# Kernel optimization log

Hardware: AMD Instinct MI355X
Metric: run time of the kernel (lower is better)

Reference implementation:

```python
import jax, jax.numpy as jnp
import numpy as np

D = 1024

def setup_inputs() -> dict:
    key = jax.random.key(0)
    ks = jax.random.split(key, 12)
    sc_in = 1.0 / np.sqrt(D)
    sc_in2 = 1.0 / np.sqrt(2 * D)
    inp = {
        "X1": jax.random.normal(ks[0], (8, D), dtype=jnp.float32),
        "X2": jax.random.normal(ks[1], (8, 2048, D), dtype=jnp.float32),
        # Linear params: weight stored as [in, out], bias [out]
        "Wq1": jax.random.normal(ks[2], (D, D), dtype=jnp.float32) * sc_in,
        "bq1": jax.random.normal(ks[3], (D,), dtype=jnp.float32) * 0.01,
        "Wq2": jax.random.normal(ks[4], (D, D), dtype=jnp.float32) * sc_in,
        "bq2": jax.random.normal(ks[5], (D,), dtype=jnp.float32) * 0.01,
        "Wk1": jax.random.normal(ks[6], (D, D), dtype=jnp.float32) * sc_in,
        "bk1": jax.random.normal(ks[7], (D,), dtype=jnp.float32) * 0.01,
        "Wk2": jax.random.normal(ks[8], (D, D), dtype=jnp.float32) * sc_in,
        "bk2": jax.random.normal(ks[9], (D,), dtype=jnp.float32) * 0.01,
        "Wv": jax.random.normal(ks[10], (2 * D, D), dtype=jnp.float32) * sc_in2,
        "bv": jax.random.normal(ks[11], (D,), dtype=jnp.float32) * 0.01,
        "alpha": jnp.float32(0.5),
    }
    return inp

def reference(X1, X2, Wq1, bq1, Wq2, bq2, Wk1, bk1, Wk2, bk2, Wv, bv, alpha):
    B, S, Dm = X2.shape
    # broadcast X1 [B, D] -> [B, S, D]
    X1e = jnp.broadcast_to(X1[:, None, :], (B, S, Dm))
    X = jnp.concatenate([X1e, X2], axis=-1)  # [B, S, 2D]
    Q1 = X1e @ Wq1 + bq1
    K1 = X1e @ Wk1 + bk1
    Q2 = X2 @ Wq2 + bq2
    K2 = X2 @ Wk2 + bk2
    V = X @ Wv + bv  # [B, S, D]
    s = 1.0 / jnp.sqrt(jnp.float32(Dm))
    A1 = jnp.einsum('bqd,bkd->bqk', Q1, K1) * s
    A2 = jnp.einsum('bqd,bkd->bqk', Q2, K2) * s
    A = jax.nn.softmax(A2, axis=-1) - alpha * jax.nn.softmax(A1, axis=-1)
    return jnp.einsum('bqk,bkd->bqd', A, V)
```

## Files before the change

### kernel.cpp

```cpp
#include <hip/hip_runtime.h>

typedef unsigned short u16;
typedef unsigned int u32;
typedef __bf16 bf16x8 __attribute__((ext_vector_type(8)));
typedef float f32x4 __attribute__((ext_vector_type(4)));
typedef u16 u16x4 __attribute__((ext_vector_type(4)));
typedef u16 u16x8 __attribute__((ext_vector_type(8)));

#define MFMA16(a,b,c) __builtin_amdgcn_mfma_f32_16x16x32_bf16((a),(b),(c),0,0,0)

__device__ __forceinline__ u16 f2bf(float f) {
  u32 u = __builtin_bit_cast(u32, f);
  u += 0x7fffu + ((u >> 16) & 1u);
  return (u16)(u >> 16);
}
__device__ __forceinline__ float bf2f(u16 h) {
  return __builtin_bit_cast(float, (u32)h << 16);
}

typedef __attribute__((address_space(1))) const void gas_void;
typedef __attribute__((address_space(3))) void las_void;
__device__ __forceinline__ void gld16(const void* g, void* l) {
  __builtin_amdgcn_global_load_lds((gas_void*)g, (las_void*)l, 16, 0, 0);
}

__global__ void init_k(float* __restrict__ p)
{
  const int i = blockIdx.x * 256 + threadIdx.x;
  ((f32x4*)p)[i] = (f32x4){0.f, 0.f, 0.f, 0.f};
}

__global__ void wtrans_k(const float* __restrict__ Wq2, const float* __restrict__ Wk2,
                         const float* __restrict__ Wv, u16* __restrict__ Tq,
                         u16* __restrict__ Tk, u16* __restrict__ Tv)
{
  __shared__ float tile[32][33];
  const float* src; u16* dst;
  if (blockIdx.z == 0)      { src = Wq2;             dst = Tq; }
  else if (blockIdx.z == 1) { src = Wk2;             dst = Tk; }
  else                      { src = Wv + 1024*1024;  dst = Tv; }
  const int k0 = blockIdx.x * 32, n0 = blockIdx.y * 32;
  const int tx = threadIdx.x, ty = threadIdx.y;
#pragma unroll
  for (int j = 0; j < 4; ++j)
    tile[ty + 8*j][tx] = src[(size_t)(k0 + ty + 8*j) * 1024 + n0 + tx];
  __syncthreads();
#pragma unroll
  for (int j = 0; j < 4; ++j)
    dst[(size_t)(n0 + ty + 8*j) * 1024 + k0 + tx] = f2bf(tile[tx][ty + 8*j]);
}

__global__ void x2bf_k(const float* __restrict__ X2, u16* __restrict__ X2b)
{
  const size_t i = ((size_t)blockIdx.x * 256 + threadIdx.x) * 8;
  f32x4 a = *(const f32x4*)(X2 + i);
  f32x4 b = *(const f32x4*)(X2 + i + 4);
  u16x8 o;
#pragma unroll
  for (int j = 0; j < 4; ++j) { o[j] = f2bf(a[j]); o[4+j] = f2bf(b[j]); }
  *(u16x8*)(X2b + i) = o;
}

__global__ void v1bv_k(const float* __restrict__ X1, const float* __restrict__ Wv,
                       const float* __restrict__ bv, float* __restrict__ v1bv)
{
  const int b = blockIdx.y, t = threadIdx.x;
  const int d = blockIdx.x * 64 + (t & 63);
  const int jg = t >> 6;
  float a = 0.f;
#pragma unroll 8
  for (int jj = 0; jj < 256; ++jj) {
    const int j = jg * 256 + jj;
    a = fmaf(X1[b*1024 + j], Wv[(size_t)j * 1024 + d], a);
  }
  __shared__ float red[256];
  red[t] = a;
  __syncthreads();
  if (t < 64)
    v1bv[b*1024 + d] = red[t] + red[t+64] + red[t+128] + red[t+192] + bv[d];
}

template<int MODE>
__global__ __launch_bounds__(512, 2) void g256(
    const u16* __restrict__ A, const u16* __restrict__ B,
    const float* __restrict__ fa, const float* __restrict__ fb,
    float* __restrict__ fm, const float* __restrict__ alphaP,
    void* __restrict__ Cout, int K)
{
  __shared__ u16 lds[65536];

  const int id = blockIdx.x;
  int b = 0, m0, n0;
  const u16 *Ab, *Bb;
  if constexpr (MODE <= 1) {
    n0 = (id & 3) * 256; m0 = (id >> 2) * 256;
    Ab = A; Bb = B;
    if constexpr (MODE == 1) b = m0 >> 11;
  } else if constexpr (MODE == 2) {
    b = id & 7; const int idx = id >> 3;
    n0 = (idx & 7) * 256; m0 = (idx >> 3) * 256;
    Ab = A + (size_t)b * 2048 * 1024;
    Bb = B + (size_t)b * 2048 * 1024;
  } else {
    b = id & 7; const int idx = id >> 3;
    n0 = (idx & 3) * 256; m0 = (idx >> 2) * 256;
    Ab = A + (size_t)b * 2048 * 2048;
    Bb = B + (size_t)b * 1024 * 2048;
  }

  const int t = threadIdx.x, lane = t & 63, w = t >> 6;
  const int wr = w >> 2, wc = w & 3;
  const int l15 = lane & 15, l4 = lane >> 4;

  const int srow = t >> 2;
  const int scolsw = (8 * (t & 3)) ^ ((srow & 6) << 2);
  const int acolsw = (l4 * 8) ^ ((l15 & 6) << 2);
  const int arow = (128 * wr + l15) * 32 + acolsw;
  const int brow = 16384 + (64 * wc + l15) * 32 + acolsw;

  const u16* A0 = Ab + (size_t)(m0 + srow) * K + scolsw;
  const u16* A1 = A0 + (size_t)128 * K;
  const u16* B0 = Bb + (size_t)(n0 + srow) * K + scolsw;
  const u16* B1 = B0 + (size_t)128 * K;

  char* ldsc = (char*)lds;
  const int wo = w * 1024;

  f32x4 acc[8][4];
#pragma unroll
  for (int i = 0; i < 8; ++i)
#pragma unroll
    for (int j = 0; j < 4; ++j) acc[i][j] = (f32x4){0.f, 0.f, 0.f, 0.f};

  gld16(A0,      ldsc + wo);
  gld16(A1,      ldsc + 8192 + wo);
  gld16(B0,      ldsc + 32768 + wo);
  gld16(B1,      ldsc + 40960 + wo);
  gld16(A0 + 32, ldsc + 16384 + wo);
  gld16(A1 + 32, ldsc + 24576 + wo);
  gld16(B0 + 32, ldsc + 49152 + wo);
  gld16(B1 + 32, ldsc + 57344 + wo);
  asm volatile("s_waitcnt vmcnt(4)" ::: "memory");
  __builtin_amdgcn_s_barrier();

  const int NKT = K >> 6;
  int cur = 0;
  for (int kt = 0; kt < NKT; ++kt) {
    const int nxt = cur ^ 1;
    const size_t koff = (size_t)(kt + 1) * 64;
    char* dst = ldsc + nxt * 65536 + wo;
    const u16* la0 = lds + cur * 32768;

    bf16x8 af[8], p0, p1;

    gld16(A0 + koff, dst);
    gld16(A1 + koff, dst + 8192);
    gld16(B0 + koff, dst + 32768);
    gld16(B1 + koff, dst + 40960);
#pragma unroll
    for (int m = 0; m < 8; ++m) af[m] = *(const bf16x8*)(la0 + arow + m * 512);
    p0 = *(const bf16x8*)(la0 + brow);
    p1 = *(const bf16x8*)(la0 + brow + 512);
    __builtin_amdgcn_s_setprio(1);
#pragma unroll
    for (int m = 0; m < 8; ++m) {
      acc[m][0] = MFMA16(af[m], p0, acc[m][0]);
      acc[m][1] = MFMA16(af[m], p1, acc[m][1]);
    }
    __builtin_amdgcn_s_setprio(0);

    gld16(A0 + koff + 32, dst + 16384);
    gld16(A1 + koff + 32, dst + 24576);
    gld16(B0 + koff + 32, dst + 49152);
    gld16(B1 + koff + 32, dst + 57344);
    p0 = *(const bf16x8*)(la0 + brow + 1024);
    p1 = *(const bf16x8*)(la0 + brow + 1536);
    __builtin_amdgcn_s_setprio(1);
#pragma unroll
    for (int m = 0; m < 8; ++m) {
      acc[m][2] = MFMA16(af[m], p0, acc[m][2]);
      acc[m][3] = MFMA16(af[m], p1, acc[m][3]);
    }
    __builtin_amdgcn_s_setprio(0);

    asm volatile("s_waitcnt vmcnt(8)" ::: "memory");
    __builtin_amdgcn_s_barrier();

#pragma unroll
    for (int m = 0; m < 8; ++m) af[m] = *(const bf16x8*)(la0 + 8192 + arow + m * 512);
    p0 = *(const bf16x8*)(la0 + 8192 + brow);
    p1 = *(const bf16x8*)(la0 + 8192 + brow + 512);
    __builtin_amdgcn_s_setprio(1);
#pragma unroll
    for (int m = 0; m < 8; ++m) {
      acc[m][0] = MFMA16(af[m], p0, acc[m][0]);
      acc[m][1] = MFMA16(af[m], p1, acc[m][1]);
    }
    __builtin_amdgcn_s_setprio(0);

    p0 = *(const bf16x8*)(la0 + 8192 + brow + 1024);
    p1 = *(const bf16x8*)(la0 + 8192 + brow + 1536);
    __builtin_amdgcn_s_setprio(1);
#pragma unroll
    for (int m = 0; m < 8; ++m) {
      acc[m][2] = MFMA16(af[m], p0, acc[m][2]);
      acc[m][3] = MFMA16(af[m], p1, acc[m][3]);
    }
    __builtin_amdgcn_s_setprio(0);

    asm volatile("s_waitcnt vmcnt(4)" ::: "memory");
    __builtin_amdgcn_s_barrier();
    cur = nxt;
  }

  if constexpr (MODE == 0) {
    u16* C = (u16*)Cout;
#pragma unroll
    for (int j = 0; j < 4; ++j) {
      const int gc = n0 + 64*wc + 16*j + l15;
      const float bb = fa[gc];
#pragma unroll
      for (int i = 0; i < 8; ++i) {
        const int gr = m0 + 128*wr + 16*i + l4*4;
#pragma unroll
        for (int r = 0; r < 4; ++r)
          C[(size_t)(gr + r) * 1024 + gc] = f2bf(acc[i][j][r] + bb);
      }
    }
  } else if constexpr (MODE == 1) {
    u16* C = (u16*)Cout;
#pragma unroll
    for (int j = 0; j < 4; ++j) {
      const int gc = n0 + 64*wc + 16*j + l15;
      const float bb = fa[b*1024 + gc];
      float colsum = 0.f;
#pragma unroll
      for (int i = 0; i < 8; ++i) {
        const int s = (m0 & 2047) + 128*wr + 16*i + l4*4;
        u16x4 pk;
#pragma unroll
        for (int r = 0; r < 4; ++r) {
          const float v = acc[i][j][r] + bb;
          pk[r] = f2bf(v);
          colsum += v;
        }
        *(u16x4*)(C + (size_t)b*1024*2048 + (size_t)gc*2048 + s) = pk;
      }
      colsum += __shfl_xor(colsum, 16);
      colsum += __shfl_xor(colsum, 32);
      if (l4 == 0) atomicAdd(&fm[b*1024 + gc], colsum);
    }
  } else if constexpr (MODE == 2) {
    u16* Cb = (u16*)Cout + (size_t)b * 2048 * 2048;
    const float scale = 0.03125f;
    float rs[8][4];
#pragma unroll
    for (int i = 0; i < 8; ++i)
#pragma unroll
      for (int r = 0; r < 4; ++r) rs[i][r] = 0.f;
#pragma unroll
    for (int j = 0; j < 4; ++j) {
      const int gc = n0 + 64*wc + 16*j + l15;
#pragma unroll
      for (int i = 0; i < 8; ++i) {
        const int gr = m0 + 128*wr + 16*i + l4*4;
#pragma unroll
        for (int r = 0; r < 4; ++r) {
          const float e = __expf(acc[i][j][r] * scale);
          rs[i][r] += e;
          Cb[(size_t)(gr + r) * 2048 + gc] = f2bf(e);
        }
      }
    }
#pragma unroll
    for (int i = 0; i < 8; ++i)
#pragma unroll
      for (int r = 0; r < 4; ++r) {
        float s = rs[i][r];
        s += __shfl_xor(s, 1);
        s += __shfl_xor(s, 2);
        s += __shfl_xor(s, 4);
        s += __shfl_xor(s, 8);
        if (l15 == 0) {
          const int gr = m0 + 128*wr + 16*i + l4*4 + r;
          atomicAdd(&fm[b*2048 + gr], s);
        }
      }
  } else {
    float* out = (float*)Cout;
    const float aS = alphaP[0] * (1.0f / 2048.0f);
    float ctv[4];
#pragma unroll
    for (int j = 0; j < 4; ++j)
      ctv[j] = aS * fb[b*1024 + n0 + 64*wc + 16*j + l15];
#pragma unroll
    for (int i = 0; i < 8; ++i) {
      const int grb = m0 + 128*wr + 16*i + l4*4;
      float li[4];
#pragma unroll
      for (int r = 0; r < 4; ++r) li[r] = 1.0f / fa[b*2048 + grb + r];
#pragma unroll
      for (int j = 0; j < 4; ++j) {
        const int gc = n0 + 64*wc + 16*j + l15;
#pragma unroll
        for (int r = 0; r < 4; ++r)
          out[(size_t)(b*2048 + grb + r) * 1024 + gc] = acc[i][j][r] * li[r] - ctv[j];
      }
    }
  }
}

extern "C" void kernel_launch(void* const* d_in, const int* in_sizes, int n_in,
                              void* d_out, int out_size, void* d_ws, size_t ws_size,
                              hipStream_t stream)
{
  const float* X1  = (const float*)d_in[0];
  const float* X2  = (const float*)d_in[1];
  const float* Wq2 = (const float*)d_in[4];
  const float* bq2 = (const float*)d_in[5];
  const float* Wk2 = (const float*)d_in[8];
  const float* bk2 = (const float*)d_in[9];
  const float* Wv  = (const float*)d_in[10];
  const float* bv  = (const float*)d_in[11];
  const float* alpha = (const float*)d_in[12];
  float* out = (float*)d_out;

  char* ws = (char*)d_ws;
  u16* Q2  = (u16*)(ws);
  u16* K2  = (u16*)(ws + 33554432);
  u16* Vt  = (u16*)(ws + 67108864);
  u16* P   = (u16*)(ws + 100663296);
  u16* X2b = (u16*)(ws + 134217728);
  u16* Tq  = (u16*)(ws + 167772160);
  u16* Tk  = (u16*)(ws + 169869312);
  u16* Tv  = (u16*)(ws + 171966464);
  float* v1bv   = (float*)(ws + 174063616);
  float* rowsum = (float*)(ws + 174096384);
  float* Vsum   = (float*)(ws + 174161920);

  init_k<<<24, 256, 0, stream>>>(rowsum);
  wtrans_k<<<dim3(32, 32, 3), dim3(32, 8), 0, stream>>>(Wq2, Wk2, Wv, Tq, Tk, Tv);
  x2bf_k<<<8192, 256, 0, stream>>>(X2, X2b);
  v1bv_k<<<dim3(16, 8), 256, 0, stream>>>(X1, Wv, bv, v1bv);

  g256<0><<<256, 512, 0, stream>>>(X2b, Tq, bq2, nullptr, nullptr, nullptr, Q2, 1024);
  g256<0><<<256, 512, 0, stream>>>(X2b, Tk, bk2, nullptr, nullptr, nullptr, K2, 1024);
  g256<1><<<256, 512, 0, stream>>>(X2b, Tv, v1bv, nullptr, Vsum, nullptr, Vt, 1024);

  g256<2><<<512, 512, 0, stream>>>(Q2, K2, nullptr, nullptr, rowsum, nullptr, P, 1024);

  g256<3><<<256, 512, 0, stream>>>(P, Vt, rowsum, Vsum, nullptr, alpha, out, 2048);
}
```

Before: 479.8 us.

## Restructure GEMM mainloop into eight-phase pipelined schedule with XOR-swizzled 64-wide LDS rows

Rewrites the shared bf16 GEMM main loop. Tiles are now stored as 64-element rows with an 8-way XOR swizzle, and each K-step is split into phases that alternate 4x4 MFMA blocks with staggered global-to-LDS loads. Each phase is fenced with barriers, lgkmcnt waits and sched_barrier, and loads are prefetched two stages ahead. Epilogues are reordered to walk rows first for better write coalescing. The aim is to hide load latency and cut LDS bank conflicts, at the cost of many more barriers per iteration and more fragile wait counts.

Result: faster. 421.3 us (-12.2%).

```diff
diff --git a/kernel.cpp b/kernel.cpp
--- a/kernel.cpp
+++ b/kernel.cpp
@@ -112,19 +112,31 @@
   const int wr = w >> 2, wc = w & 3;
   const int l15 = lane & 15, l4 = lane >> 4;
 
-  const int srow = t >> 2;
-  const int scolsw = (8 * (t & 3)) ^ ((srow & 6) << 2);
-  const int acolsw = (l4 * 8) ^ ((l15 & 6) << 2);
-  const int arow = (128 * wr + l15) * 32 + acolsw;
-  const int brow = 16384 + (64 * wc + l15) * 32 + acolsw;
-
-  const u16* A0 = Ab + (size_t)(m0 + srow) * K + scolsw;
-  const u16* A1 = A0 + (size_t)128 * K;
-  const u16* B0 = Bb + (size_t)(n0 + srow) * K + scolsw;
-  const u16* B1 = B0 + (size_t)128 * K;
-
+  const int cs0 = (l4 ^ (l15 & 7)) * 8;
+  const int cs1 = ((4 + l4) ^ (l15 & 7)) * 8;
+  const int aBase = wr * 8192 + l15 * 64;
+  const int bBase = 32768 + (wc >> 1) * 8192 + (wc & 1) * 4096 + l15 * 64;
+
+  const int srow = t >> 3;
+  const int scol = ((t & 7) ^ (srow & 7)) * 8;
+  const u16* As = Ab + (size_t)(m0 + srow) * K + scol;
+  const u16* Bs = Bb + (size_t)(n0 + srow) * K + scol;
   char* ldsc = (char*)lds;
-  const int wo = w * 1024;
+  const int wdst = w * 1024;
+  const int NKT = K >> 6;
+
+  auto stA = [&](int s, int h) {
+    const size_t ro = (size_t)(128 * h) * K + (size_t)s * 64;
+    char* d = ldsc + (s & 1) * 32768 + h * 16384 + wdst;
+    gld16(As + ro, d);
+    gld16(As + ro + (size_t)64 * K, d + 8192);
+  };
+  auto stB = [&](int s, int h) {
+    const size_t ro = (size_t)(128 * h) * K + (size_t)s * 64;
+    char* d = ldsc + 65536 + (s & 1) * 32768 + h * 16384 + wdst;
+    gld16(Bs + ro, d);
+    gld16(Bs + ro + (size_t)64 * K, d + 8192);
+  };
 
   f32x4 acc[8][4];
 #pragma unroll
@@ -132,101 +144,93 @@
 #pragma unroll
     for (int j = 0; j < 4; ++j) acc[i][j] = (f32x4){0.f, 0.f, 0.f, 0.f};
 
-  gld16(A0,      ldsc + wo);
-  gld16(A1,      ldsc + 8192 + wo);
-  gld16(B0,      ldsc + 32768 + wo);
-  gld16(B1,      ldsc + 40960 + wo);
-  gld16(A0 + 32, ldsc + 16384 + wo);
-  gld16(A1 + 32, ldsc + 24576 + wo);
-  gld16(B0 + 32, ldsc + 49152 + wo);
-  gld16(B1 + 32, ldsc + 57344 + wo);
-  asm volatile("s_waitcnt vmcnt(4)" ::: "memory");
+  bf16x8 af[4], bfr[4];
+  auto rdA = [&](int buf, int mlo, int kkcs) {
+    const int base = buf * 16384 + aBase + kkcs;
+#pragma unroll
+    for (int m = 0; m < 4; ++m)
+      af[m] = *(const bf16x8*)&lds[base + (mlo + m) * 1024];
+  };
+  auto rdB = [&](int buf, int kkcs) {
+    const int base = buf * 16384 + bBase + kkcs;
+#pragma unroll
+    for (int j = 0; j < 4; ++j)
+      bfr[j] = *(const bf16x8*)&lds[base + j * 1024];
+  };
+  auto mm = [&](int mlo) {
+#pragma unroll
+    for (int m = 0; m < 4; ++m)
+#pragma unroll
+      for (int j = 0; j < 4; ++j)
+        acc[mlo + m][j] = MFMA16(af[m], bfr[j], acc[mlo + m][j]);
+  };
+
+#define PH_MID                                              \
+  __builtin_amdgcn_s_barrier();                             \
+  asm volatile("s_waitcnt lgkmcnt(0)" ::: "memory");        \
+  __builtin_amdgcn_sched_barrier(0);                        \
+  __builtin_amdgcn_s_setprio(1);
+#define PH_END                                              \
+  __builtin_amdgcn_s_setprio(0);                            \
   __builtin_amdgcn_s_barrier();
-
-  const int NKT = K >> 6;
-  int cur = 0;
-  for (int kt = 0; kt < NKT; ++kt) {
-    const int nxt = cur ^ 1;
-    const size_t koff = (size_t)(kt + 1) * 64;
-    char* dst = ldsc + nxt * 65536 + wo;
-    const u16* la0 = lds + cur * 32768;
-
-    bf16x8 af[8], p0, p1;
-
-    gld16(A0 + koff, dst);
-    gld16(A1 + koff, dst + 8192);
-    gld16(B0 + koff, dst + 32768);
-    gld16(B1 + koff, dst + 40960);
-#pragma unroll
-    for (int m = 0; m < 8; ++m) af[m] = *(const bf16x8*)(la0 + arow + m * 512);
-    p0 = *(const bf16x8*)(la0 + brow);
-    p1 = *(const bf16x8*)(la0 + brow + 512);
-    __builtin_amdgcn_s_setprio(1);
-#pragma unroll
-    for (int m = 0; m < 8; ++m) {
-      acc[m][0] = MFMA16(af[m], p0, acc[m][0]);
-      acc[m][1] = MFMA16(af[m], p1, acc[m][1]);
-    }
-    __builtin_amdgcn_s_setprio(0);
-
-    gld16(A0 + koff + 32, dst + 16384);
-    gld16(A1 + koff + 32, dst + 24576);
-    gld16(B0 + koff + 32, dst + 49152);
-    gld16(B1 + koff + 32, dst + 57344);
-    p0 = *(const bf16x8*)(la0 + brow + 1024);
-    p1 = *(const bf16x8*)(la0 + brow + 1536);
-    __builtin_amdgcn_s_setprio(1);
-#pragma unroll
-    for (int m = 0; m < 8; ++m) {
-      acc[m][2] = MFMA16(af[m], p0, acc[m][2]);
-      acc[m][3] = MFMA16(af[m], p1, acc[m][3]);
-    }
-    __builtin_amdgcn_s_setprio(0);
-
-    asm volatile("s_waitcnt vmcnt(8)" ::: "memory");
-    __builtin_amdgcn_s_barrier();
-
-#pragma unroll
-    for (int m = 0; m < 8; ++m) af[m] = *(const bf16x8*)(la0 + 8192 + arow + m * 512);
-    p0 = *(const bf16x8*)(la0 + 8192 + brow);
-    p1 = *(const bf16x8*)(la0 + 8192 + brow + 512);
-    __builtin_amdgcn_s_setprio(1);
-#pragma unroll
-    for (int m = 0; m < 8; ++m) {
-      acc[m][0] = MFMA16(af[m], p0, acc[m][0]);
-      acc[m][1] = MFMA16(af[m], p1, acc[m][1]);
-    }
-    __builtin_amdgcn_s_setprio(0);
-
-    p0 = *(const bf16x8*)(la0 + 8192 + brow + 1024);
-    p1 = *(const bf16x8*)(la0 + 8192 + brow + 1536);
-    __builtin_amdgcn_s_setprio(1);
-#pragma unroll
-    for (int m = 0; m < 8; ++m) {
-      acc[m][2] = MFMA16(af[m], p0, acc[m][2]);
-      acc[m][3] = MFMA16(af[m], p1, acc[m][3]);
-    }
-    __builtin_amdgcn_s_setprio(0);
-
-    asm volatile("s_waitcnt vmcnt(4)" ::: "memory");
-    __builtin_amdgcn_s_barrier();
-    cur = nxt;
+#define PH_ENDV                                             \
+  __builtin_amdgcn_s_setprio(0);                            \
+  asm volatile("s_waitcnt vmcnt(2)" ::: "memory");          \
+  __builtin_amdgcn_sched_barrier(0);                        \
+  __builtin_amdgcn_s_barrier();
+
+  stA(0, 0); stA(0, 1); stB(0, 0); stB(0, 1);
+  stB(1, 0);
+  asm volatile("s_waitcnt vmcnt(2)" ::: "memory");
+  __builtin_amdgcn_sched_barrier(0);
+  __builtin_amdgcn_s_barrier();
+
+  const int NI = NKT >> 1;
+  for (int i = 0; i < NI; ++i) {
+    const int T = 2 * i;
+    const int s1 = T + 1;
+    const int s2 = (T + 2 < NKT) ? T + 2 : NKT - 1;
+    const int s3 = (T + 3 < NKT) ? T + 3 : NKT - 1;
+
+    rdA(0, 0, cs0); rdB(0, cs0); stB(s1, 1);
+    PH_MID; mm(0); PH_END;
+    rdA(0, 4, cs0); stA(s1, 0);
+    PH_MID; mm(4); PH_END;
+    rdA(0, 0, cs1); rdB(0, cs1); stA(s1, 1);
+    PH_MID; mm(0); PH_END;
+    rdA(0, 4, cs1); stB(s2, 0);
+    PH_MID; mm(4); PH_ENDV;
+
+    rdA(1, 0, cs0); rdB(1, cs0); stA(s2, 0);
+    PH_MID; mm(0); PH_END;
+    rdA(1, 4, cs0); stA(s2, 1);
+    PH_MID; mm(4); PH_END;
+    rdA(1, 0, cs1); rdB(1, cs1); stB(s2, 1);
+    PH_MID; mm(0); PH_END;
+    rdA(1, 4, cs1); stB(s3, 0);
+    PH_MID; mm(4); PH_ENDV;
   }
+  asm volatile("s_waitcnt vmcnt(0)" ::: "memory");
+#undef PH_MID
+#undef PH_END
+#undef PH_ENDV
 
   if constexpr (MODE == 0) {
     u16* C = (u16*)Cout;
-#pragma unroll
-    for (int j = 0; j < 4; ++j) {
-      const int gc = n0 + 64*wc + 16*j + l15;
-      const float bb = fa[gc];
-#pragma unroll
-      for (int i = 0; i < 8; ++i) {
-        const int gr = m0 + 128*wr + 16*i + l4*4;
-#pragma unroll
-        for (int r = 0; r < 4; ++r)
-          C[(size_t)(gr + r) * 1024 + gc] = f2bf(acc[i][j][r] + bb);
-      }
-    }
+    float bb[4];
+#pragma unroll
+    for (int j = 0; j < 4; ++j) bb[j] = fa[n0 + 64*wc + 16*j + l15];
+#pragma unroll
+    for (int i = 0; i < 8; ++i)
+#pragma unroll
+      for (int r = 0; r < 4; ++r) {
+        const int gr = m0 + 128*wr + 16*i + l4*4 + r;
+#pragma unroll
+        for (int j = 0; j < 4; ++j) {
+          const int gc = n0 + 64*wc + 16*j + l15;
+          C[(size_t)gr * 1024 + gc] = f2bf(acc[i][j][r] + bb[j]);
+        }
+      }
   } else if constexpr (MODE == 1) {
     u16* C = (u16*)Cout;
 #pragma unroll
@@ -253,30 +257,23 @@
   } else if constexpr (MODE == 2) {
     u16* Cb = (u16*)Cout + (size_t)b * 2048 * 2048;
     const float scale = 0.03125f;
-    float rs[8][4];
-#pragma unroll
-    for (int i = 0; i < 8; ++i)
-#pragma unroll
-      for (int r = 0; r < 4; ++r) rs[i][r] = 0.f;
-#pragma unroll
-    for (int j = 0; j < 4; ++j) {
-      const int gc = n0 + 64*wc + 16*j + l15;
-#pragma unroll
-      for (int i = 0; i < 8; ++i) {
-        const int gr = m0 + 128*wr + 16*i + l4*4;
-#pragma unroll
-        for (int r = 0; r < 4; ++r) {
+#pragma unroll
+    for (int i = 0; i < 8; ++i) {
+      float rs[4] = {0.f, 0.f, 0.f, 0.f};
+#pragma unroll
+      for (int r = 0; r < 4; ++r) {
+        const int gr = m0 + 128*wr + 16*i + l4*4 + r;
+#pragma unroll
+        for (int j = 0; j < 4; ++j) {
+          const int gc = n0 + 64*wc + 16*j + l15;
           const float e = __expf(acc[i][j][r] * scale);
-          rs[i][r] += e;
-          Cb[(size_t)(gr + r) * 2048 + gc] = f2bf(e);
-        }
-      }
-    }
-#pragma unroll
-    for (int i = 0; i < 8; ++i)
+          rs[r] += e;
+          Cb[(size_t)gr * 2048 + gc] = f2bf(e);
+        }
+      }
 #pragma unroll
       for (int r = 0; r < 4; ++r) {
-        float s = rs[i][r];
+        float s = rs[r];
         s += __shfl_xor(s, 1);
         s += __shfl_xor(s, 2);
         s += __shfl_xor(s, 4);
@@ -286,6 +283,7 @@
           atomicAdd(&fm[b*2048 + gr], s);
         }
       }
+    }
   } else {
     float* out = (float*)Cout;
     const float aS = alphaP[0] * (1.0f / 2048.0f);
@@ -295,16 +293,15 @@
       ctv[j] = aS * fb[b*1024 + n0 + 64*wc + 16*j + l15];
 #pragma unroll
     for (int i = 0; i < 8; ++i) {
-      const int grb = m0 + 128*wr + 16*i + l4*4;
-      float li[4];
-#pragma unroll
-      for (int r = 0; r < 4; ++r) li[r] = 1.0f / fa[b*2048 + grb + r];
-#pragma unroll
-      for (int j = 0; j < 4; ++j) {
-        const int gc = n0 + 64*wc + 16*j + l15;
-#pragma unroll
-        for (int r = 0; r < 4; ++r)
-          out[(size_t)(b*2048 + grb + r) * 1024 + gc] = acc[i][j][r] * li[r] - ctv[j];
+#pragma unroll
+      for (int r = 0; r < 4; ++r) {
+        const int gr = m0 + 128*wr + 16*i + l4*4 + r;
+        const float li = 1.0f / fa[b*2048 + gr];
+#pragma unroll
+        for (int j = 0; j < 4; ++j) {
+          const int gc = n0 + 64*wc + 16*j + l15;
+          out[(size_t)(b*2048 + gr) * 1024 + gc] = acc[i][j][r] * li - ctv[j];
+        }
       }
     }
   }
```
